# Kernel optimization log

Hardware: AMD Instinct MI355X
Metric: run time of the kernel (lower is better)

Reference implementation:

```python
import jax, jax.numpy as jnp
import numpy as np

NUM_HEADS = 16

def rotate_half(x):
    x1, x2 = jnp.split(x, 2, axis=-1)
    return jnp.concatenate((-x2, x1), axis=-1)

def setup_inputs() -> dict:
    key = jax.random.key(0)
    ks = jax.random.split(key, 5)
    b, n, dim, hd = 2, 2048, 1024, 64
    return {
        "x": jax.random.normal(ks[0], (b, n, dim), dtype=jnp.float32),
        "Wqkv": jax.random.normal(ks[1], (3 * dim, dim), dtype=jnp.float32) * (dim ** -0.5),
        "Wproj": jax.random.normal(ks[2], (dim, dim), dtype=jnp.float32) * (dim ** -0.5),
        "bproj": jnp.zeros((dim,), dtype=jnp.float32),
        "sin": jax.random.normal(ks[3], (n, hd), dtype=jnp.float32),
        "cos": jax.random.normal(ks[4], (n, hd), dtype=jnp.float32),
    }

def reference(x, Wqkv, Wproj, bproj, sin, cos):
    b, n, dim = x.shape
    h = NUM_HEADS
    d = dim // h
    qkv = x @ Wqkv.T
    qkv = qkv.reshape(b, n, 3, h, d).transpose(2, 0, 3, 1, 4)
    q, k, v = qkv[0], qkv[1], qkv[2]
    # RoPE: sin/cos [n, d] broadcast over [b, h, n, d]
    q = q * cos + rotate_half(q) * sin
    k = k * cos + rotate_half(k) * sin
    # SDPA (non-causal, no dropout at eval)
    scale = d ** -0.5
    scores = jnp.einsum("bhnd,bhmd->bhnm", q, k) * scale
    attn = jax.nn.softmax(scores, axis=-1)
    out = jnp.einsum("bhnm,bhmd->bhnd", attn, v)
    # merge heads: [b, h, n, d] -> [b, n, h*d]
    out = out.transpose(0, 2, 1, 3).reshape(b, n, dim)
    return out @ Wproj.T + bproj
```

## Files before the change

### kernel.cpp

```cpp
#include <hip/hip_runtime.h>
#include <hip/hip_fp16.h>

typedef _Float16 f16;
typedef _Float16 half8 __attribute__((ext_vector_type(8)));
typedef _Float16 half4v __attribute__((ext_vector_type(4)));
typedef float f32x4 __attribute__((ext_vector_type(4)));

#define QSCALE 0.18033688011112042f
#define SHIFT2 17.312340490667560f

__device__ __forceinline__ void gload_lds16(const void* g, void* lds) {
  __builtin_amdgcn_global_load_lds(
      (__attribute__((address_space(1))) void*)g,
      (__attribute__((address_space(3))) void*)lds, 16, 0, 0);
}

__global__ __launch_bounds__(256) void cvt_f32_f16_kernel(
    const float* __restrict__ src, f16* __restrict__ dst, int n4) {
  int i = blockIdx.x * 256 + threadIdx.x;
  if (i >= n4) return;
  float4 v = ((const float4*)src)[i];
  half4v o;
  o.x = (f16)v.x; o.y = (f16)v.y; o.z = (f16)v.z; o.w = (f16)v.w;
  ((half4v*)dst)[i] = o;
}

template<int EPI>
__global__ __launch_bounds__(256) void hgemm_kernel(
    const f16* __restrict__ A16, const f16* __restrict__ B, int K,
    const float* __restrict__ cosT, const float* __restrict__ sinT,
    f16* __restrict__ Qout, f16* __restrict__ Kout, f16* __restrict__ Vtout,
    const float* __restrict__ bias, float* __restrict__ Cout) {
  __shared__ f16 As[2][128 * 32];
  __shared__ f16 Bs[2][64 * 32];
  const int tid = threadIdx.x;
  const int lane = tid & 63, w = tid >> 6;
  const int fr = lane & 15, fkg = lane >> 4, fk = fkg * 8;
  const int wm = (w >> 1) * 64, wn2 = (w & 1) * 16;
  const long long rowBase = (long long)blockIdx.x * 128;
  const long long colBase = (long long)blockIdx.y * 64;

  f32x4 acc[4][2] = {};
  const f16* Ab = A16 + rowBase * K;
  const f16* Bb = B + colBase * K;

  auto stage = [&](int buf, int k0) {
#pragma unroll
    for (int r = 0; r < 2; ++r) {
      int c = r * 4 + w;
      int off = (c * 64 + lane) * 8;
      int row = off >> 5, col = off & 31;
      gload_lds16(Ab + (long long)row * K + k0 + col, &As[buf][c * 512]);
    }
    {
      int off = (w * 64 + lane) * 8;
      int row = off >> 5, col = off & 31;
      gload_lds16(Bb + (long long)row * K + k0 + col, &Bs[buf][w * 512]);
    }
  };

  stage(0, 0);
  for (int k0 = 0; k0 < K; k0 += 32) {
    const int buf = (k0 >> 5) & 1;
    __syncthreads();
    if (k0 + 32 < K) stage(buf ^ 1, k0 + 32);
    half8 a[4], b[2];
#pragma unroll
    for (int i = 0; i < 4; ++i)
      a[i] = *(const half8*)(&As[buf][(wm + i * 16 + fr) * 32 + fk]);
#pragma unroll
    for (int j = 0; j < 2; ++j)
      b[j] = *(const half8*)(&Bs[buf][(wn2 + j * 32 + fr) * 32 + fk]);
#pragma unroll
    for (int i = 0; i < 4; ++i)
#pragma unroll
      for (int j = 0; j < 2; ++j)
        acc[i][j] = __builtin_amdgcn_mfma_f32_16x16x32_f16(a[i], b[j], acc[i][j], 0, 0, 0);
  }

  if (EPI == 0) {
#pragma unroll
    for (int i = 0; i < 4; ++i) {
#pragma unroll
      for (int r = 0; r < 4; ++r) {
        int rg = (int)rowBase + wm + i * 16 + fkg * 4 + r;
        int bidx = rg >> 11, nn = rg & 2047;
#pragma unroll
        for (int j = 0; j < 2; ++j) {
          int cg = (int)colBase + wn2 + j * 32 + fr;
          int t = cg >> 10, cc = cg & 1023;
          int head = cc >> 6, d = cc & 63;
          int bh = bidx * 16 + head;
          float v = acc[i][j][r];
          if (t == 2) {
            Vtout[((long long)bh * 64 + d) * 2048 + nn] = (f16)v;
          } else {
            float pal = acc[i][j ^ 1][r];
            float cs = cosT[nn * 64 + d];
            float sn = sinT[nn * 64 + d];
            v = v * cs + (d < 32 ? -pal : pal) * sn;
            if (t == 0) v *= QSCALE;
            f16 hv = (f16)v;
            if (t == 0) Qout[((long long)bh * 2048 + nn) * 64 + d] = hv;
            else        Kout[((long long)bh * 2048 + nn) * 64 + d] = hv;
          }
        }
      }
    }
  } else {
#pragma unroll
    for (int i = 0; i < 4; ++i)
#pragma unroll
      for (int r = 0; r < 4; ++r) {
        long long rg = rowBase + wm + i * 16 + fkg * 4 + r;
#pragma unroll
        for (int j = 0; j < 2; ++j) {
          int cg = (int)colBase + wn2 + j * 32 + fr;
          Cout[rg * 1024 + cg] = acc[i][j][r] + bias[cg];
        }
      }
  }
}

__global__ __launch_bounds__(256) void attn_kernel(
    const f16* __restrict__ Q, const f16* __restrict__ Kb,
    const f16* __restrict__ Vt, f16* __restrict__ Om) {
  __shared__ f16 Ks[64 * 72];
  __shared__ f16 Vs[64 * 72];
  __shared__ f16 Ps[4][32 * 72];
  const int tid = threadIdx.x;
  const int lane = tid & 63, w = tid >> 6;
  const int fr = lane & 15, fkg = lane >> 4, fk = fkg * 8;
  const int bh = blockIdx.y;
  const int q0 = blockIdx.x * 128 + w * 32;
  f16* Psw = &Ps[w][0];

  half8 aq[2][2];
#pragma unroll
  for (int m = 0; m < 2; ++m)
#pragma unroll
    for (int ks = 0; ks < 2; ++ks)
      aq[m][ks] = *(const half8*)(Q + ((long long)bh * 2048 + q0 + m * 16 + fr) * 64 +
                                  ks * 32 + fk);

  half8 ones_frag;
#pragma unroll
  for (int j = 0; j < 8; ++j) ones_frag[j] = (fr == 0) ? (f16)1.0f : (f16)0.0f;

  f32x4 acc[2][5] = {};

  const int soff = tid * 8;
  const int skr0 = soff >> 6, sd0 = soff & 63;
  half8 kreg[2], vreg[2];
#pragma unroll
  for (int c = 0; c < 2; ++c) {
    int kr = skr0 + c * 32;
    kreg[c] = *(const half8*)(Kb + ((long long)bh * 2048 + kr) * 64 + sd0);
    vreg[c] = *(const half8*)(Vt + ((long long)bh * 64 + kr) * 2048 + sd0);
  }

  for (int kv0 = 0; kv0 < 2048; kv0 += 64) {
    __syncthreads();
#pragma unroll
    for (int c = 0; c < 2; ++c) {
      int kr = skr0 + c * 32;
      *(half8*)(Ks + kr * 72 + sd0) = kreg[c];
      *(half8*)(Vs + kr * 72 + sd0) = vreg[c];
    }
    if (kv0 + 64 < 2048) {
#pragma unroll
      for (int c = 0; c < 2; ++c) {
        int kr = skr0 + c * 32;
        kreg[c] = *(const half8*)(Kb + ((long long)bh * 2048 + kv0 + 64 + kr) * 64 + sd0);
        vreg[c] = *(const half8*)(Vt + ((long long)bh * 64 + kr) * 2048 + kv0 + 64 + sd0);
      }
    }
    __syncthreads();

    f32x4 z[2][4];
#pragma unroll
    for (int n = 0; n < 4; ++n) {
      half8 bk0 = *(const half8*)(Ks + (n * 16 + fr) * 72 + fk);
      half8 bk1 = *(const half8*)(Ks + (n * 16 + fr) * 72 + 32 + fk);
#pragma unroll
      for (int m = 0; m < 2; ++m) {
        f32x4 t = {0.f, 0.f, 0.f, 0.f};
        t = __builtin_amdgcn_mfma_f32_16x16x32_f16(bk0, aq[m][0], t, 0, 0, 0);
        t = __builtin_amdgcn_mfma_f32_16x16x32_f16(bk1, aq[m][1], t, 0, 0, 0);
        z[m][n] = t;
      }
    }

#pragma unroll
    for (int m = 0; m < 2; ++m)
#pragma unroll
      for (int n = 0; n < 4; ++n) {
        half4v h;
#pragma unroll
        for (int r = 0; r < 4; ++r)
          h[r] = (f16)__builtin_amdgcn_exp2f(z[m][n][r] - SHIFT2);
        *(half4v*)(Psw + (m * 16 + fr) * 72 + n * 16 + fkg * 4) = h;
      }

#pragma unroll
    for (int ks = 0; ks < 2; ++ks) {
      half8 ap[2];
#pragma unroll
      for (int m = 0; m < 2; ++m) {
        ap[m] = *(const half8*)(Psw + (m * 16 + fr) * 72 + ks * 32 + fk);
        acc[m][4] = __builtin_amdgcn_mfma_f32_16x16x32_f16(ap[m], ones_frag, acc[m][4], 0, 0, 0);
      }
#pragma unroll
      for (int dd = 0; dd < 4; ++dd) {
        half8 bv = *(const half8*)(Vs + (dd * 16 + fr) * 72 + ks * 32 + fk);
#pragma unroll
        for (int m = 0; m < 2; ++m)
          acc[m][dd] = __builtin_amdgcn_mfma_f32_16x16x32_f16(ap[m], bv, acc[m][dd], 0, 0, 0);
      }
    }
  }

  const int b = bh >> 4, h = bh & 15;
#pragma unroll
  for (int m = 0; m < 2; ++m)
#pragma unroll
    for (int r = 0; r < 4; ++r) {
      int nn = q0 + m * 16 + fkg * 4 + r;
      float l = __shfl(acc[m][4][r], lane & 48);
      float inv = 1.f / l;
#pragma unroll
      for (int dd = 0; dd < 4; ++dd)
        Om[((long long)b * 2048 + nn) * 1024 + h * 64 + dd * 16 + fr] =
            (f16)(acc[m][dd][r] * inv);
    }
}

extern "C" void kernel_launch(void* const* d_in, const int* in_sizes, int n_in,
                              void* d_out, int out_size, void* d_ws, size_t ws_size,
                              hipStream_t stream) {
  (void)in_sizes; (void)n_in; (void)out_size; (void)ws_size;
  const float* x     = (const float*)d_in[0];
  const float* Wqkv  = (const float*)d_in[1];
  const float* Wproj = (const float*)d_in[2];
  const float* bproj = (const float*)d_in[3];
  const float* sinT  = (const float*)d_in[4];
  const float* cosT  = (const float*)d_in[5];
  float* out = (float*)d_out;

  f16* ws     = (f16*)d_ws;
  f16* xh     = ws;
  f16* Om     = ws;
  f16* Wqkvh  = ws + 4194304;
  f16* Wprojh = ws + 7340032;
  f16* Qb     = ws + 8388608;
  f16* Kb     = ws + 12582912;
  f16* Vtb    = ws + 16777216;

  cvt_f32_f16_kernel<<<4096, 256, 0, stream>>>(x, xh, 1048576);
  cvt_f32_f16_kernel<<<3072, 256, 0, stream>>>(Wqkv, Wqkvh, 786432);
  cvt_f32_f16_kernel<<<1024, 256, 0, stream>>>(Wproj, Wprojh, 262144);

  hgemm_kernel<0><<<dim3(32, 48), 256, 0, stream>>>(
      xh, Wqkvh, 1024, cosT, sinT, Qb, Kb, Vtb, nullptr, nullptr);

  attn_kernel<<<dim3(16, 32), 256, 0, stream>>>(Qb, Kb, Vtb, Om);

  hgemm_kernel<1><<<dim3(32, 16), 256, 0, stream>>>(
      Om, Wprojh, 1024, nullptr, nullptr, nullptr, nullptr, nullptr, bproj, out);
}
```

Before: 140.7 us.

## Widen QKV GEMM tile to 128 columns and use MFMA-fragment LDS layout

The QKV projection GEMM now uses a 128x128 block tile with each wave computing 64x64, halving the grid in the column dimension and doubling B-operand reuse per A load. The LDS staging layout is changed so each 16-row by 32-k chunk is stored in MFMA fragment order, which makes the global-to-LDS loads and the fragment reads line up and is meant to cut bank conflicts. The RoPE partner lookup changes to j^2 to match the new column mapping. More accumulators per thread raise register pressure, and the smaller grid may occupy the CUs less well.

```diff
diff --git a/kernel.cpp b/kernel.cpp
--- a/kernel.cpp
+++ b/kernel.cpp
@@ -31,31 +31,40 @@
     const float* __restrict__ cosT, const float* __restrict__ sinT,
     f16* __restrict__ Qout, f16* __restrict__ Kout, f16* __restrict__ Vtout,
     const float* __restrict__ bias, float* __restrict__ Cout) {
+  constexpr int BN = (EPI == 0) ? 128 : 64;
+  constexpr int NJ = (EPI == 0) ? 4 : 2;
   __shared__ f16 As[2][128 * 32];
-  __shared__ f16 Bs[2][64 * 32];
+  __shared__ f16 Bs[2][BN * 32];
   const int tid = threadIdx.x;
   const int lane = tid & 63, w = tid >> 6;
-  const int fr = lane & 15, fkg = lane >> 4, fk = fkg * 8;
-  const int wm = (w >> 1) * 64, wn2 = (w & 1) * 16;
+  const int fr = lane & 15, fkg = lane >> 4;
+  const int wm = (w >> 1) * 64;
+  const int wn = (EPI == 0) ? (w & 1) * 64 : (w & 1) * 16;
   const long long rowBase = (long long)blockIdx.x * 128;
-  const long long colBase = (long long)blockIdx.y * 64;
-
-  f32x4 acc[4][2] = {};
+  const long long colBase = (long long)blockIdx.y * BN;
+
+  f32x4 acc[4][NJ] = {};
   const f16* Ab = A16 + rowBase * K;
   const f16* Bb = B + colBase * K;
 
+  const int sr = lane & 15;
+  const int sq = (lane >> 4) * 8;
+
   auto stage = [&](int buf, int k0) {
 #pragma unroll
     for (int r = 0; r < 2; ++r) {
       int c = r * 4 + w;
-      int off = (c * 64 + lane) * 8;
-      int row = off >> 5, col = off & 31;
-      gload_lds16(Ab + (long long)row * K + k0 + col, &As[buf][c * 512]);
-    }
-    {
-      int off = (w * 64 + lane) * 8;
-      int row = off >> 5, col = off & 31;
-      gload_lds16(Bb + (long long)row * K + k0 + col, &Bs[buf][w * 512]);
+      gload_lds16(Ab + (long long)(c * 16 + sr) * K + k0 + sq, &As[buf][c * 512]);
+    }
+    if (EPI == 0) {
+#pragma unroll
+      for (int r = 0; r < 2; ++r) {
+        int c = r * 4 + w;
+        gload_lds16(Bb + (long long)(c * 16 + sr) * K + k0 + sq, &Bs[buf][c * 512]);
+      }
+    } else {
+      int c = w;
+      gload_lds16(Bb + (long long)(c * 16 + sr) * K + k0 + sq, &Bs[buf][c * 512]);
     }
   };
 
@@ -64,17 +73,21 @@
     const int buf = (k0 >> 5) & 1;
     __syncthreads();
     if (k0 + 32 < K) stage(buf ^ 1, k0 + 32);
-    half8 a[4], b[2];
+    half8 a[4], b[NJ];
+#pragma unroll
+    for (int i = 0; i < 4; ++i) {
+      int row = wm + i * 16 + fr;
+      a[i] = *(const half8*)(&As[buf][((row >> 4) << 9) + (fkg << 7) + ((row & 15) << 3)]);
+    }
+#pragma unroll
+    for (int j = 0; j < NJ; ++j) {
+      int row = (EPI == 0) ? (wn + j * 16 + fr) : (wn + j * 32 + fr);
+      b[j] = *(const half8*)(&Bs[buf][((row >> 4) << 9) + (fkg << 7) + ((row & 15) << 3)]);
+    }
 #pragma unroll
     for (int i = 0; i < 4; ++i)
-      a[i] = *(const half8*)(&As[buf][(wm + i * 16 + fr) * 32 + fk]);
-#pragma unroll
-    for (int j = 0; j < 2; ++j)
-      b[j] = *(const half8*)(&Bs[buf][(wn2 + j * 32 + fr) * 32 + fk]);
-#pragma unroll
-    for (int i = 0; i < 4; ++i)
-#pragma unroll
-      for (int j = 0; j < 2; ++j)
+#pragma unroll
+      for (int j = 0; j < NJ; ++j)
         acc[i][j] = __builtin_amdgcn_mfma_f32_16x16x32_f16(a[i], b[j], acc[i][j], 0, 0, 0);
   }
 
@@ -86,8 +99,8 @@
         int rg = (int)rowBase + wm + i * 16 + fkg * 4 + r;
         int bidx = rg >> 11, nn = rg & 2047;
 #pragma unroll
-        for (int j = 0; j < 2; ++j) {
-          int cg = (int)colBase + wn2 + j * 32 + fr;
+        for (int j = 0; j < 4; ++j) {
+          int cg = (int)colBase + wn + j * 16 + fr;
           int t = cg >> 10, cc = cg & 1023;
           int head = cc >> 6, d = cc & 63;
           int bh = bidx * 16 + head;
@@ -95,7 +108,7 @@
           if (t == 2) {
             Vtout[((long long)bh * 64 + d) * 2048 + nn] = (f16)v;
           } else {
-            float pal = acc[i][j ^ 1][r];
+            float pal = acc[i][j ^ 2][r];
             float cs = cosT[nn * 64 + d];
             float sn = sinT[nn * 64 + d];
             v = v * cs + (d < 32 ? -pal : pal) * sn;
@@ -114,8 +127,8 @@
       for (int r = 0; r < 4; ++r) {
         long long rg = rowBase + wm + i * 16 + fkg * 4 + r;
 #pragma unroll
-        for (int j = 0; j < 2; ++j) {
-          int cg = (int)colBase + wn2 + j * 32 + fr;
+        for (int j = 0; j < NJ; ++j) {
+          int cg = (int)colBase + wn + j * 32 + fr;
           Cout[rg * 1024 + cg] = acc[i][j][r] + bias[cg];
         }
       }
@@ -260,7 +273,7 @@
   cvt_f32_f16_kernel<<<3072, 256, 0, stream>>>(Wqkv, Wqkvh, 786432);
   cvt_f32_f16_kernel<<<1024, 256, 0, stream>>>(Wproj, Wprojh, 262144);
 
-  hgemm_kernel<0><<<dim3(32, 48), 256, 0, stream>>>(
+  hgemm_kernel<0><<<dim3(32, 24), 256, 0, stream>>>(
       xh, Wqkvh, 1024, cosT, sinT, Qb, Kb, Vtb, nullptr, nullptr);
 
   attn_kernel<<<dim3(16, 32), 256, 0, stream>>>(Qb, Kb, Vtb, Om);
```

New measurement: 159.0 us. +13.1%, slower.
